# Kernel tuning notes

Measured on AMD Instinct MI355X. Metric: run time of the kernel, lower is better.

Reference implementation:

```python
import jax, jax.numpy as jnp
import numpy as np
from jax import lax

B, T, J, C = 256, 512, 25, 3
IN_DIM = J * C  # 75
H = 256


def gru_layer(x, W_ih, W_hh, b_ih, b_hh):
    """PyTorch-semantics GRU layer. x: [B,T,Din] -> (out [B,T,H], h_T [B,H]).
    Gate order in stacked weights: r, z, n (PyTorch convention)."""
    Hh = W_hh.shape[1]
    # precompute input contributions for all timesteps
    xg = jnp.einsum('bti,gi->btg', x, W_ih) + b_ih  # [B,T,3H]

    def step(h, xg_t):
        hg = h @ W_hh.T + b_hh  # [B,3H]
        xr, xz, xn = jnp.split(xg_t, 3, axis=-1)
        hr, hz, hn = jnp.split(hg, 3, axis=-1)
        r = jax.nn.sigmoid(xr + hr)
        z = jax.nn.sigmoid(xz + hz)
        n = jnp.tanh(xn + r * hn)
        h_new = (1.0 - z) * n + z * h
        return h_new, h_new

    h0 = jnp.zeros((x.shape[0], Hh), x.dtype)
    hT, outs = lax.scan(step, h0, jnp.swapaxes(xg, 0, 1))  # scan over time
    return jnp.swapaxes(outs, 0, 1), hT


def setup_inputs() -> dict:
    key = jax.random.key(0)
    ks = jax.random.split(key, 12)
    s_in = 1.0 / np.sqrt(H)

    def u(k, shape):
        return jax.random.uniform(k, shape, jnp.float32, -s_in, s_in)

    return {
        'x': jax.random.normal(ks[0], (B, T, J, C), jnp.float32),
        'W_ih0': u(ks[1], (3 * H, IN_DIM)),
        'W_hh0': u(ks[2], (3 * H, H)),
        'b_ih0': u(ks[3], (3 * H,)),
        'b_hh0': u(ks[4], (3 * H,)),
        'W_ih1': u(ks[5], (3 * H, H)),
        'W_hh1': u(ks[6], (3 * H, H)),
        'b_ih1': u(ks[7], (3 * H,)),
        'b_hh1': u(ks[8], (3 * H,)),
        'fc_W': u(ks[9], (H, H)),
        'fc_b': u(ks[10], (H,)),
    }


def reference(x, W_ih0, W_hh0, b_ih0, b_hh0, W_ih1, W_hh1, b_ih1, b_hh1, fc_W, fc_b):
    b, t, j, c = x.shape
    xf = x.reshape(b, t, j * 3)  # matches torch view(B, T, J*3)
    out0, _ = gru_layer(xf, W_ih0, W_hh0, b_ih0, b_hh0)
    _, hT = gru_layer(out0, W_ih1, W_hh1, b_ih1, b_hh1)
    # unidirectional: final hidden state of last layer -> fc
    embedding = hT @ fc_W.T + fc_b  # [B, H]
    return embedding
```

## Files before the change

### kernel.cpp

```cpp
#include <hip/hip_runtime.h>
#include <hip/hip_bf16.h>
#include <stdint.h>
#include <stddef.h>


typedef _Float16 f16;
typedef _Float16 f16x8 __attribute__((ext_vector_type(8)));
typedef _Float16 f16x4 __attribute__((ext_vector_type(4)));
typedef float    f32x4 __attribute__((ext_vector_type(4)));

#define B_      256
#define T_      512
#define H_      256
#define G_      768
#define IN_RAW  75
#define KX      96
#define MROWS   (T_*B_)

__device__ __forceinline__ float sigm(float x){ return 1.f/(1.f+__expf(-x)); }
__device__ __forceinline__ float tanh_(float x){ return 1.f - 2.f/(1.f+__expf(2.f*x)); }

__device__ __forceinline__ void bar_lds(){
  asm volatile("s_waitcnt lgkmcnt(0)" ::: "memory");
  __builtin_amdgcn_s_barrier();
  __builtin_amdgcn_sched_barrier(0);
}

__global__ __launch_bounds__(256) void cast_x(const float* __restrict__ x,
                                              f16* __restrict__ xb){
  int idx = blockIdx.x*256 + threadIdx.x;
  int row = idx / KX;
  int j   = idx - row*KX;
  int t   = row >> 8;
  int b   = row & 255;
  float v = (j < IN_RAW) ? x[((size_t)b*T_ + t)*IN_RAW + j] : 0.f;
  xb[idx] = (f16)v;
}

__global__ __launch_bounds__(256) void cast_w(
    const float* __restrict__ Wih0, const float* __restrict__ Whh0,
    const float* __restrict__ Wih1, const float* __restrict__ Whh1,
    const float* __restrict__ fcW,
    const float* __restrict__ bih0, const float* __restrict__ bhh0,
    const float* __restrict__ bih1, const float* __restrict__ bhh1,
    f16* __restrict__ W0h, f16* __restrict__ Whh0h, f16* __restrict__ Wih1h,
    f16* __restrict__ Whh1h, f16* __restrict__ fcWh,
    float* __restrict__ bias0, float* __restrict__ bias1){
  int i = blockIdx.x*256 + threadIdx.x;
  if (i < 73728){ int r = i/KX, j = i - r*KX;
    W0h[i] = (f16)((j < IN_RAW) ? Wih0[r*IN_RAW + j] : 0.f); return; }
  i -= 73728;
  if (i < 196608){ Whh0h[i] = (f16)Whh0[i]; return; } i -= 196608;
  if (i < 196608){ Wih1h[i] = (f16)Wih1[i]; return; } i -= 196608;
  if (i < 196608){ Whh1h[i] = (f16)Whh1[i]; return; } i -= 196608;
  if (i < 65536){ fcWh[i] = (f16)fcW[i]; return; } i -= 65536;
  if (i < 768){ bias0[i] = bih0[i] + (i < 512 ? bhh0[i] : 0.f); return; } i -= 768;
  if (i < 768){ bias1[i] = bih1[i] + (i < 512 ? bhh1[i] : 0.f); }
}

__global__ __launch_bounds__(256) void cast_h(const float* __restrict__ hs,
                                              f16* __restrict__ hT){
  int i = blockIdx.x*256 + threadIdx.x;
  hT[i] = (f16)hs[i];
}

template<int K, int BN, bool OUTF32>
__global__ __launch_bounds__(256, 2) void gemm_k(const f16* __restrict__ A,
    const f16* __restrict__ W, const float* __restrict__ bias,
    void* __restrict__ outp, const int N){
  constexpr int NT = BN/16;
  const int tid  = threadIdx.x;
  const int wave = tid >> 6, lane = tid & 63;
  const int quad = lane >> 4, l16 = lane & 15;
  const long mbase = (long)blockIdx.x*128 + wave*32;
  const int  nbase = blockIdx.y*BN;
  f32x4 acc[2][NT] = {};
#pragma unroll 2
  for (int kc = 0; kc < K/32; ++kc){
    f16x8 a0 = *(const f16x8*)(A + (mbase +      l16)*K + kc*32 + quad*8);
    f16x8 a1 = *(const f16x8*)(A + (mbase + 16 + l16)*K + kc*32 + quad*8);
#pragma unroll
    for (int nt = 0; nt < NT; ++nt){
      f16x8 b = *(const f16x8*)(W + (long)(nbase + nt*16 + l16)*K + kc*32 + quad*8);
      acc[0][nt] = __builtin_amdgcn_mfma_f32_16x16x32_f16(a0, b, acc[0][nt], 0, 0, 0);
      acc[1][nt] = __builtin_amdgcn_mfma_f32_16x16x32_f16(a1, b, acc[1][nt], 0, 0, 0);
    }
  }
#pragma unroll
  for (int nt = 0; nt < NT; ++nt){
    const int col = nbase + nt*16 + l16;
    const float bv = bias[col];
#pragma unroll
    for (int af = 0; af < 2; ++af){
#pragma unroll
      for (int r = 0; r < 4; ++r){
        const long row = mbase + af*16 + quad*4 + r;
        float v = acc[af][nt][r] + bv;
        if (OUTF32) ((float*)outp)[row*(long)N + col] = v;
        else        ((f16*)outp)[row*(long)N + col] = (f16)v;
      }
    }
  }
}

template<int K>
__device__ __forceinline__ void gemm_body128(const f16* __restrict__ A,
    const f16* __restrict__ W, const float* __restrict__ bias,
    f16* __restrict__ out, const int bx, const int by){
  const int tid  = threadIdx.x;
  const int wave = tid >> 6, lane = tid & 63;
  const int quad = lane >> 4, l16 = lane & 15;
  const int nbase = by*128;
#pragma unroll
  for (int mt = 0; mt < 2; ++mt){
    const long mbase = (long)bx*512 + mt*256 + wave*32;
    f32x4 acc[2][8] = {};
#pragma unroll 2
    for (int kc = 0; kc < K/32; ++kc){
      f16x8 a0 = *(const f16x8*)(A + (mbase +      l16)*K + kc*32 + quad*8);
      f16x8 a1 = *(const f16x8*)(A + (mbase + 16 + l16)*K + kc*32 + quad*8);
#pragma unroll
      for (int nt = 0; nt < 8; ++nt){
        f16x8 b = *(const f16x8*)(W + (long)(nbase + nt*16 + l16)*K + kc*32 + quad*8);
        acc[0][nt] = __builtin_amdgcn_mfma_f32_16x16x32_f16(a0, b, acc[0][nt], 0, 0, 0);
        acc[1][nt] = __builtin_amdgcn_mfma_f32_16x16x32_f16(a1, b, acc[1][nt], 0, 0, 0);
      }
    }
#pragma unroll
    for (int nt = 0; nt < 8; ++nt){
      const int col = nbase + nt*16 + l16;
      const float bv = bias[col];
#pragma unroll
      for (int af = 0; af < 2; ++af)
#pragma unroll
        for (int r = 0; r < 4; ++r)
          out[(mbase + af*16 + quad*4 + r)*(long)G_ + col] = (f16)(acc[af][nt][r] + bv);
    }
  }
}

__device__ __forceinline__ void scan_body(const f16* __restrict__ xg,
    const f16* __restrict__ Whh, const float* __restrict__ bhh,
    float* __restrict__ hstate, f16* __restrict__ out0,
    const int TC, const int bx){
  __shared__ char  hbufB[2][16*512];
  __shared__ f16   nlds[65536];
  __shared__ float bnlds[256];
  const int tid  = threadIdx.x;
  const int wave = tid >> 6, lane = tid & 63;
  const int quad = lane >> 4, l16 = lane & 15;
  const int b0   = bx*16;
  const int jj   = wave*32 + quad*4;

  f16x8 w[2][2][8];
#pragma unroll
  for (int s = 0; s < 2; ++s)
#pragma unroll
    for (int g = 0; g < 2; ++g)
#pragma unroll
      for (int kc = 0; kc < 8; ++kc)
        w[s][g][kc] = *(const f16x8*)(Whh + (size_t)(g*256 + wave*32 + s*16 + l16)*H_ + kc*32 + quad*8);
#pragma unroll
  for (int s = 0; s < 2; ++s)
#pragma unroll
    for (int g = 0; g < 2; ++g)
#pragma unroll
      for (int kc = 0; kc < 8; ++kc)
        asm volatile("" : "+a"(w[s][g][kc]));

#pragma unroll
  for (int i = 0; i < 16; ++i){
    const int p  = i*512 + tid;
    const int f  = p >> 6, L = p & 63;
    const int wv = f >> 4, ss = (f >> 3) & 1, kcc = f & 7;
    const int row = 512 + wv*32 + ss*16 + (L & 15);
    const int k   = kcc*32 + (L >> 4)*8;
    *(f16x8*)&nlds[(size_t)p*8] = *(const f16x8*)(Whh + (size_t)row*H_ + k);
  }
  if (tid < 256) bnlds[tid] = bhh[512 + tid];

  f32x4 h[2];
#pragma unroll
  for (int s = 0; s < 2; ++s){
    h[s] = *(const f32x4*)(hstate + (size_t)(b0 + l16)*H_ + jj + s*16);
    f16x4 hh;
#pragma unroll
    for (int r = 0; r < 4; ++r) hh[r] = (f16)h[s][r];
    const int ch = wave*4 + s*2 + (quad>>1);
    *(f16x4*)&hbufB[0][l16*512 + ((ch ^ (l16&7))<<4) + ((quad&1)<<3)] = hh;
  }

  const f16* xgl = xg + (size_t)(b0 + l16)*G_ + jj;
  f16x4 cur[6];
#pragma unroll
  for (int s = 0; s < 2; ++s)
#pragma unroll
    for (int g = 0; g < 3; ++g)
      cur[s*3+g] = *(const f16x4*)(xgl + g*256 + s*16);

  __syncthreads();

  for (int t = 0; t < TC; ++t){
    const int pb = t & 1;
    f32x4 acc[2][3] = {};
#pragma unroll
    for (int kc = 0; kc < 8; ++kc){
      f16x8 hf = *(const f16x8*)&hbufB[pb][l16*512 + ((((kc<<2)|quad) ^ (l16&7))<<4)];
#pragma unroll
      for (int s = 0; s < 2; ++s){
        acc[s][0] = __builtin_amdgcn_mfma_f32_16x16x32_f16(w[s][0][kc], hf, acc[s][0], 0,0,0);
        acc[s][1] = __builtin_amdgcn_mfma_f32_16x16x32_f16(w[s][1][kc], hf, acc[s][1], 0,0,0);
        f16x8 nf = *(const f16x8*)&nlds[(size_t)(((wave<<4)|(s<<3)|kc)*64 + lane)*8];
        acc[s][2] = __builtin_amdgcn_mfma_f32_16x16x32_f16(nf, hf, acc[s][2], 0,0,0);
      }
    }
    f16x4 hh[2];
#pragma unroll
    for (int s = 0; s < 2; ++s){
      const f32x4 bnv = *(const f32x4*)&bnlds[jj + s*16];
#pragma unroll
      for (int r = 0; r < 4; ++r){
        float rg = sigm((float)cur[s*3+0][r] + acc[s][0][r]);
        float zg = sigm((float)cur[s*3+1][r] + acc[s][1][r]);
        float ng = tanh_((float)cur[s*3+2][r] + rg*(acc[s][2][r] + bnv[r]));
        float hv = (1.f - zg)*ng + zg*h[s][r];
        h[s][r] = hv;
        hh[s][r] = (f16)hv;
      }
    }
    if (t+1 < TC){
      const f16* xn_ = xgl + (size_t)(t+1)*(B_*G_);
#pragma unroll
      for (int s = 0; s < 2; ++s)
#pragma unroll
        for (int g = 0; g < 3; ++g)
          cur[s*3+g] = *(const f16x4*)(xn_ + g*256 + s*16);
    }
#pragma unroll
    for (int s = 0; s < 2; ++s){
      const int ch = wave*4 + s*2 + (quad>>1);
      *(f16x4*)&hbufB[pb^1][l16*512 + ((ch ^ (l16&7))<<4) + ((quad&1)<<3)] = hh[s];
      if (out0)
        *(f16x4*)(out0 + ((size_t)t*B_ + b0 + l16)*H_ + jj + s*16) = hh[s];
    }
    bar_lds();
  }

#pragma unroll
  for (int s = 0; s < 2; ++s)
    *(f32x4*)(hstate + (size_t)(b0 + l16)*H_ + jj + s*16) = h[s];
}

__global__ __launch_bounds__(512)
__attribute__((amdgpu_waves_per_eu(2, 2)))
void fused(
    const f16* __restrict__ xg0, const f16* __restrict__ Whh0,
    const float* __restrict__ bhh0, float* __restrict__ h0s,
    f16* __restrict__ out0w,
    const f16* __restrict__ xg1, const f16* __restrict__ Whh1,
    const float* __restrict__ bhh1, float* __restrict__ h1s,
    const f16* __restrict__ g0A, const f16* __restrict__ g0W,
    const float* __restrict__ g0b, f16* __restrict__ g0out,
    const f16* __restrict__ g1A, const f16* __restrict__ g1W,
    const float* __restrict__ g1b, f16* __restrict__ g1out,
    const int TC, const int mask){
  const int bid = blockIdx.x;
  if (bid < 16){
    if (!(mask & 1)) return;
    scan_body(xg0, Whh0, bhh0, h0s, out0w, TC, bid);
  } else if (bid < 32){
    if (!(mask & 2)) return;
    scan_body(xg1, Whh1, bhh1, h1s, (f16*)nullptr, TC, bid - 16);
  } else {
    int g = bid - 32;
    const int RB = TC/2;
    if (g < 3*TC){
      if (!(mask & 4)) return;
      gemm_body128<96>(g0A, g0W, g0b, g0out, g % RB, g / RB);
    } else {
      g -= 3*TC;
      if (!(mask & 8)) return;
      gemm_body128<256>(g1A, g1W, g1b, g1out, g % RB, g / RB);
    }
  }
}

extern "C" void kernel_launch(void* const* d_in, const int* in_sizes, int n_in,
                              void* d_out, int out_size, void* d_ws, size_t ws_size,
                              hipStream_t stream){
  (void)in_sizes; (void)n_in; (void)out_size;
  const float* x    = (const float*)d_in[0];
  const float* Wih0 = (const float*)d_in[1];
  const float* Whh0 = (const float*)d_in[2];
  const float* bih0 = (const float*)d_in[3];
  const float* bhh0 = (const float*)d_in[4];
  const float* Wih1 = (const float*)d_in[5];
  const float* Whh1 = (const float*)d_in[6];
  const float* bih1 = (const float*)d_in[7];
  const float* bhh1 = (const float*)d_in[8];
  const float* fcW  = (const float*)d_in[9];
  const float* fcb  = (const float*)d_in[10];

  char* ws = (char*)d_ws;
  size_t off = 0;
  auto alloc = [&](size_t bytes) -> void* {
    void* p = ws + off; off += (bytes + 255) & ~(size_t)255; return p;
  };
  f16*   xb    = (f16*)  alloc((size_t)MROWS*KX*2);
  f16*   W0h   = (f16*)  alloc((size_t)G_*KX*2);
  f16*   Whh0h = (f16*)  alloc((size_t)G_*H_*2);
  f16*   Wih1h = (f16*)  alloc((size_t)G_*H_*2);
  f16*   Whh1h = (f16*)  alloc((size_t)G_*H_*2);
  f16*   fcWh  = (f16*)  alloc((size_t)H_*H_*2);
  float* bias0 = (float*)alloc(G_*4);
  float* bias1 = (float*)alloc(G_*4);
  float* h0s   = (float*)alloc((size_t)B_*H_*4);
  float* h1s   = (float*)alloc((size_t)B_*H_*4);
  f16*   hTh   = (f16*)  alloc((size_t)B_*H_*2);
  const size_t fixed = off;

  int TC = 32;
  while (TC > 8 && fixed + (size_t)TC*1835008 + 1024 > ws_size) TC >>= 1;
  f16* xg0[2], *xg1[2], *out0[2];
  xg0[0]  = (f16*)alloc((size_t)TC*B_*G_*2);
  xg0[1]  = (f16*)alloc((size_t)TC*B_*G_*2);
  xg1[0]  = (f16*)alloc((size_t)TC*B_*G_*2);
  xg1[1]  = (f16*)alloc((size_t)TC*B_*G_*2);
  out0[0] = (f16*)alloc((size_t)TC*B_*H_*2);
  out0[1] = (f16*)alloc((size_t)TC*B_*H_*2);
  const int nc = T_ / TC;

  hipMemsetAsync(h0s, 0, (size_t)B_*H_*4*2, stream);
  hipLaunchKernelGGL(cast_x, dim3(49152), dim3(256), 0, stream, x, xb);
  hipLaunchKernelGGL(cast_w, dim3(2854), dim3(256), 0, stream,
                     Wih0, Whh0, Wih1, Whh1, fcW, bih0, bhh0, bih1, bhh1,
                     W0h, Whh0h, Wih1h, Whh1h, fcWh, bias0, bias1);

  hipLaunchKernelGGL((gemm_k<96,192,false>), dim3(TC*2,4), dim3(256), 0, stream,
                     xb, W0h, bias0, (void*)xg0[0], G_);

  const dim3 grid(32 + 6*TC);
  for (int i = 0; i <= nc + 1; ++i){
    int mask = 0;
    if (i < nc)            mask |= 1;
    if (i >= 2)            mask |= 2;
    if (i + 1 < nc)        mask |= 4;
    if (i >= 1 && i <= nc) mask |= 8;
    hipLaunchKernelGGL(fused, grid, dim3(512), 0, stream,
                       xg0[i&1], Whh0h, bhh0, h0s, out0[i&1],
                       xg1[i&1], Whh1h, bhh1, h1s,
                       xb + (size_t)(i+1)*TC*B_*KX, W0h, bias0, xg0[(i+1)&1],
                       out0[(i+1)&1], Wih1h, bias1, xg1[(i+1)&1],
                       TC, mask);
  }

  hipLaunchKernelGGL(cast_h, dim3(256), dim3(256), 0, stream, h1s, hTh);
  hipLaunchKernelGGL((gemm_k<256,64,true>), dim3(2,4), dim3(256), 0, stream,
                     hTh, fcWh, fcb, d_out, H_);
}
```

Measured before the change: 1.921 ms.

## Process 32 batch rows per scan block, halving scan blocks and reusing weights

Each recurrent scan block now handles two 16-row batch chunks, so the register-resident and LDS-resident W_hh fragments are reused across both chunks. This halves the scan block count from 32 to 16 and doubles the MFMA work per step. The double-buffered h buffer becomes a single buffer guarded by two barriers per step, and xg loads for the current step move after the MFMAs instead of being prefetched. The n-gate bias is folded into the accumulator init, and the h update uses one fewer multiply. The cost is a longer serial chain per step, fewer CUs running the scan, and an extra barrier per timestep.

```diff
diff --git a/kernel.cpp b/kernel.cpp
--- a/kernel.cpp
+++ b/kernel.cpp
@@ -143,13 +143,12 @@
     const f16* __restrict__ Whh, const float* __restrict__ bhh,
     float* __restrict__ hstate, f16* __restrict__ out0,
     const int TC, const int bx){
-  __shared__ char  hbufB[2][16*512];
-  __shared__ f16   nlds[65536];
-  __shared__ float bnlds[256];
+  __shared__ f16  nlds[65536];
+  __shared__ char hbufB[16384];
   const int tid  = threadIdx.x;
   const int wave = tid >> 6, lane = tid & 63;
   const int quad = lane >> 4, l16 = lane & 15;
-  const int b0   = bx*16;
+  const int b0   = bx*32;
   const int jj   = wave*32 + quad*4;
 
   f16x8 w[2][2][8];
@@ -177,78 +176,101 @@
     const int k   = kcc*32 + (L >> 4)*8;
     *(f16x8*)&nlds[(size_t)p*8] = *(const f16x8*)(Whh + (size_t)row*H_ + k);
   }
-  if (tid < 256) bnlds[tid] = bhh[512 + tid];
-
-  f32x4 h[2];
-#pragma unroll
-  for (int s = 0; s < 2; ++s){
-    h[s] = *(const f32x4*)(hstate + (size_t)(b0 + l16)*H_ + jj + s*16);
-    f16x4 hh;
-#pragma unroll
-    for (int r = 0; r < 4; ++r) hh[r] = (f16)h[s][r];
-    const int ch = wave*4 + s*2 + (quad>>1);
-    *(f16x4*)&hbufB[0][l16*512 + ((ch ^ (l16&7))<<4) + ((quad&1)<<3)] = hh;
-  }
+
+  f32x4 bnv[2];
+#pragma unroll
+  for (int s = 0; s < 2; ++s)
+    bnv[s] = *(const f32x4*)(bhh + 512 + jj + s*16);
+
+  f32x4 h[2][2];
+#pragma unroll
+  for (int bc = 0; bc < 2; ++bc)
+#pragma unroll
+    for (int s = 0; s < 2; ++s){
+      h[bc][s] = *(const f32x4*)(hstate + (size_t)(b0 + bc*16 + l16)*H_ + jj + s*16);
+      f16x4 hh;
+#pragma unroll
+      for (int r = 0; r < 4; ++r) hh[r] = (f16)h[bc][s][r];
+      const int ch = wave*4 + s*2 + (quad>>1);
+      *(f16x4*)&hbufB[(bc*16 + l16)*512 + ((ch ^ (l16&7))<<4) + ((quad&1)<<3)] = hh;
+    }
 
   const f16* xgl = xg + (size_t)(b0 + l16)*G_ + jj;
-  f16x4 cur[6];
-#pragma unroll
-  for (int s = 0; s < 2; ++s)
-#pragma unroll
-    for (int g = 0; g < 3; ++g)
-      cur[s*3+g] = *(const f16x4*)(xgl + g*256 + s*16);
+  f16* o0l = out0 ? out0 + (size_t)(b0 + l16)*H_ + jj : (f16*)nullptr;
 
   __syncthreads();
 
+#pragma unroll 1
   for (int t = 0; t < TC; ++t){
-    const int pb = t & 1;
-    f32x4 acc[2][3] = {};
+    f32x4 acc[2][2][3];
+#pragma unroll
+    for (int bc = 0; bc < 2; ++bc)
+#pragma unroll
+      for (int s = 0; s < 2; ++s){
+        acc[bc][s][0] = (f32x4){0.f,0.f,0.f,0.f};
+        acc[bc][s][1] = (f32x4){0.f,0.f,0.f,0.f};
+        acc[bc][s][2] = bnv[s];
+      }
 #pragma unroll
     for (int kc = 0; kc < 8; ++kc){
-      f16x8 hf = *(const f16x8*)&hbufB[pb][l16*512 + ((((kc<<2)|quad) ^ (l16&7))<<4)];
+      const int sw = (((kc<<2)|quad) ^ (l16&7))<<4;
+      f16x8 hf0 = *(const f16x8*)&hbufB[ l16      *512 + sw];
+      f16x8 hf1 = *(const f16x8*)&hbufB[(l16 + 16)*512 + sw];
 #pragma unroll
       for (int s = 0; s < 2; ++s){
-        acc[s][0] = __builtin_amdgcn_mfma_f32_16x16x32_f16(w[s][0][kc], hf, acc[s][0], 0,0,0);
-        acc[s][1] = __builtin_amdgcn_mfma_f32_16x16x32_f16(w[s][1][kc], hf, acc[s][1], 0,0,0);
         f16x8 nf = *(const f16x8*)&nlds[(size_t)(((wave<<4)|(s<<3)|kc)*64 + lane)*8];
-        acc[s][2] = __builtin_amdgcn_mfma_f32_16x16x32_f16(nf, hf, acc[s][2], 0,0,0);
-      }
-    }
-    f16x4 hh[2];
-#pragma unroll
-    for (int s = 0; s < 2; ++s){
-      const f32x4 bnv = *(const f32x4*)&bnlds[jj + s*16];
-#pragma unroll
-      for (int r = 0; r < 4; ++r){
-        float rg = sigm((float)cur[s*3+0][r] + acc[s][0][r]);
-        float zg = sigm((float)cur[s*3+1][r] + acc[s][1][r]);
-        float ng = tanh_((float)cur[s*3+2][r] + rg*(acc[s][2][r] + bnv[r]));
-        float hv = (1.f - zg)*ng + zg*h[s][r];
-        h[s][r] = hv;
-        hh[s][r] = (f16)hv;
-      }
-    }
-    if (t+1 < TC){
-      const f16* xn_ = xgl + (size_t)(t+1)*(B_*G_);
+        acc[0][s][0] = __builtin_amdgcn_mfma_f32_16x16x32_f16(w[s][0][kc], hf0, acc[0][s][0], 0,0,0);
+        acc[1][s][0] = __builtin_amdgcn_mfma_f32_16x16x32_f16(w[s][0][kc], hf1, acc[1][s][0], 0,0,0);
+        acc[0][s][1] = __builtin_amdgcn_mfma_f32_16x16x32_f16(w[s][1][kc], hf0, acc[0][s][1], 0,0,0);
+        acc[1][s][1] = __builtin_amdgcn_mfma_f32_16x16x32_f16(w[s][1][kc], hf1, acc[1][s][1], 0,0,0);
+        acc[0][s][2] = __builtin_amdgcn_mfma_f32_16x16x32_f16(nf, hf0, acc[0][s][2], 0,0,0);
+        acc[1][s][2] = __builtin_amdgcn_mfma_f32_16x16x32_f16(nf, hf1, acc[1][s][2], 0,0,0);
+      }
+    }
+    f16x4 cur[2][6];
+    const f16* xt = xgl + (size_t)t*(B_*G_);
+#pragma unroll
+    for (int bc = 0; bc < 2; ++bc)
 #pragma unroll
       for (int s = 0; s < 2; ++s)
 #pragma unroll
         for (int g = 0; g < 3; ++g)
-          cur[s*3+g] = *(const f16x4*)(xn_ + g*256 + s*16);
-    }
-#pragma unroll
-    for (int s = 0; s < 2; ++s){
-      const int ch = wave*4 + s*2 + (quad>>1);
-      *(f16x4*)&hbufB[pb^1][l16*512 + ((ch ^ (l16&7))<<4) + ((quad&1)<<3)] = hh[s];
-      if (out0)
-        *(f16x4*)(out0 + ((size_t)t*B_ + b0 + l16)*H_ + jj + s*16) = hh[s];
-    }
+          cur[bc][s*3+g] = *(const f16x4*)(xt + bc*16*G_ + g*256 + s*16);
+
     bar_lds();
-  }
-
-#pragma unroll
-  for (int s = 0; s < 2; ++s)
-    *(f32x4*)(hstate + (size_t)(b0 + l16)*H_ + jj + s*16) = h[s];
+
+    f16x4 hh[2][2];
+#pragma unroll
+    for (int bc = 0; bc < 2; ++bc)
+#pragma unroll
+      for (int s = 0; s < 2; ++s){
+#pragma unroll
+        for (int r = 0; r < 4; ++r){
+          float rg = sigm((float)cur[bc][s*3+0][r] + acc[bc][s][0][r]);
+          float zg = sigm((float)cur[bc][s*3+1][r] + acc[bc][s][1][r]);
+          float ng = tanh_((float)cur[bc][s*3+2][r] + rg*acc[bc][s][2][r]);
+          float hv = ng + zg*(h[bc][s][r] - ng);
+          h[bc][s][r] = hv;
+          hh[bc][s][r] = (f16)hv;
+        }
+        const int ch = wave*4 + s*2 + (quad>>1);
+        *(f16x4*)&hbufB[(bc*16 + l16)*512 + ((ch ^ (l16&7))<<4) + ((quad&1)<<3)] = hh[bc][s];
+      }
+    if (o0l){
+#pragma unroll
+      for (int bc = 0; bc < 2; ++bc)
+#pragma unroll
+        for (int s = 0; s < 2; ++s)
+          *(f16x4*)(o0l + ((size_t)t*B_ + bc*16)*H_ + s*16) = hh[bc][s];
+    }
+    bar_lds();
+  }
+
+#pragma unroll
+  for (int bc = 0; bc < 2; ++bc)
+#pragma unroll
+    for (int s = 0; s < 2; ++s)
+      *(f32x4*)(hstate + (size_t)(b0 + bc*16 + l16)*H_ + jj + s*16) = h[bc][s];
 }
 
 __global__ __launch_bounds__(512)
@@ -265,14 +287,14 @@
     const float* __restrict__ g1b, f16* __restrict__ g1out,
     const int TC, const int mask){
   const int bid = blockIdx.x;
-  if (bid < 16){
+  if (bid < 8){
     if (!(mask & 1)) return;
     scan_body(xg0, Whh0, bhh0, h0s, out0w, TC, bid);
-  } else if (bid < 32){
+  } else if (bid < 16){
     if (!(mask & 2)) return;
-    scan_body(xg1, Whh1, bhh1, h1s, (f16*)nullptr, TC, bid - 16);
+    scan_body(xg1, Whh1, bhh1, h1s, (f16*)nullptr, TC, bid - 8);
   } else {
-    int g = bid - 32;
+    int g = bid - 16;
     const int RB = TC/2;
     if (g < 3*TC){
       if (!(mask & 4)) return;
@@ -339,7 +361,7 @@
   hipLaunchKernelGGL((gemm_k<96,192,false>), dim3(TC*2,4), dim3(256), 0, stream,
                      xb, W0h, bias0, (void*)xg0[0], G_);
 
-  const dim3 grid(32 + 6*TC);
+  const dim3 grid(16 + 6*TC);
   for (int i = 0; i <= nc + 1; ++i){
     int mask = 0;
     if (i < nc)            mask |= 1;
```

Result: slower. 4.791 ms (+149.4%).
